# Optimization experiments

Measured on AMD Instinct MI355X. Metric: run time of the kernel, lower is better.

The kernel has to match this reference:

```python
import jax, jax.numpy as jnp
import numpy as np

B, S, D = 4096, 200, 64
EPS = 1e-3  # keras BatchNormalization default epsilon

def setup_inputs() -> dict:
    key = jax.random.key(0)
    ks = jax.random.split(key, 8)
    return {
        "em": jax.random.normal(ks[0], (B, D), jnp.float32),
        "eu": jax.random.normal(ks[1], (B, D), jnp.float32),
        "Xu": jax.random.normal(ks[2], (B, S, D), jnp.float32),
        "W1": jax.random.normal(ks[3], (4 * D, 64), jnp.float32) * 0.05,
        "b1": jnp.zeros((64,), jnp.float32),
        "W2": jax.random.normal(ks[4], (64, 32), jnp.float32) * 0.1,
        "b2": jnp.zeros((32,), jnp.float32),
        "W3": jax.random.normal(ks[5], (32, 1), jnp.float32) * 0.1,
        "b3": jnp.zeros((1,), jnp.float32),
        "gamma": jnp.ones((2 * D,), jnp.float32),
        "beta": jnp.zeros((2 * D,), jnp.float32),
        "mov_mean": jnp.zeros((2 * D,), jnp.float32),
        "mov_var": jnp.ones((2 * D,), jnp.float32),
    }

def reference(em, eu, Xu, W1, b1, W2, b2, W3, b3, gamma, beta, mov_mean, mov_var):
    # DIN attention: query = em tiled over seq, key = value = Xu
    q = jnp.broadcast_to(em[:, None, :], Xu.shape)            # [B,S,D]
    info = jnp.concatenate([q, Xu, q - Xu, q * Xu], axis=-1)  # [B,S,4D]
    h = jax.nn.relu(info @ W1 + b1)                           # [B,S,64]
    h = jax.nn.relu(h @ W2 + b2)                              # [B,S,32]
    logits = (h @ W3 + b3)[..., 0]                            # [B,S]
    w = jax.nn.softmax(logits, axis=-1)                       # [B,S]
    pooled = jnp.einsum('bs,bsd->bd', w, Xu)                  # [B,D]
    info_all = jnp.concatenate([pooled, em], axis=-1)         # [B,2D]
    bn = (info_all - mov_mean) * jax.lax.rsqrt(mov_var + EPS) * gamma + beta
    return jnp.concatenate([bn, eu], axis=-1)                 # [B,2D+Du]
```

## Files before the change

kernel.cpp:

```cpp
#include <hip/hip_runtime.h>
#include <hip/hip_bf16.h>
#include <math.h>

typedef __bf16 bf16_t;
typedef bf16_t bf16x2 __attribute__((ext_vector_type(2)));
typedef bf16_t bf16x8 __attribute__((ext_vector_type(8)));
typedef float  f32x4  __attribute__((ext_vector_type(4)));
typedef int    i32x4  __attribute__((ext_vector_type(4)));
typedef unsigned int u32;

#define SEQ 200
#define DD  64

#define MFMA(a, b, c) __builtin_amdgcn_mfma_f32_16x16x32_bf16((a), (b), (c), 0, 0, 0)

__global__ __launch_bounds__(256) void prep_kernel(
    const float* __restrict__ W1, const float* __restrict__ W2,
    bf16_t* __restrict__ Wbc, bf16_t* __restrict__ W1dt,
    bf16_t* __restrict__ W2t, float* __restrict__ W1sT)
{
  const int tid = threadIdx.x;
  for (int i = tid; i < 64 * 64; i += 256) {
    int n = i >> 6, k = i & 63;
    Wbc[i]  = (bf16_t)(W1[(64 + k) * 64 + n] - W1[(128 + k) * 64 + n]);
    W1dt[i] = (bf16_t)(W1[(192 + k) * 64 + n]);
    W1sT[i] = W1[k * 64 + n] + W1[(128 + k) * 64 + n];
  }
  for (int i = tid; i < 32 * 64; i += 256) {
    int n = i >> 6, k = i & 63;
    W2t[i] = (bf16_t)(W2[k * 32 + n]);
  }
}

__device__ __forceinline__ u32 pk2(float x, float y) {
  bf16x2 t;
  t[0] = (bf16_t)fmaxf(x, 0.f);
  t[1] = (bf16_t)fmaxf(y, 0.f);
  return __builtin_bit_cast(u32, t);
}

#define XR4(v) { v += __shfl_xor(v, 1); v += __shfl_xor(v, 2); \
                 v += __shfl_xor(v, 4); v += __shfl_xor(v, 8); }
#define XM4(v) { v = fmaxf(v, __shfl_xor(v, 1)); v = fmaxf(v, __shfl_xor(v, 2)); \
                 v = fmaxf(v, __shfl_xor(v, 4)); v = fmaxf(v, __shfl_xor(v, 8)); }

#define LOADT(t, Y0, Y1, Y2, Y3) do {                                          \
    int row_ = 16 * (t) + l16;                                                 \
    row_ = row_ < SEQ ? row_ : (SEQ - 1);                                      \
    const float4* p_ = Xr + (row_ * 16 + 2 * g);                               \
    Y0 = p_[0]; Y1 = p_[1]; Y2 = p_[8]; Y3 = p_[9];                            \
  } while (0)

#define PROC(MASKED, Y0, Y1, Y2, Y3) do {                                      \
    bf16x8 a0_, a1_;                                                           \
    a0_[0]=(bf16_t)Y0.x; a0_[1]=(bf16_t)Y0.y; a0_[2]=(bf16_t)Y0.z; a0_[3]=(bf16_t)Y0.w; \
    a0_[4]=(bf16_t)Y1.x; a0_[5]=(bf16_t)Y1.y; a0_[6]=(bf16_t)Y1.z; a0_[7]=(bf16_t)Y1.w; \
    a1_[0]=(bf16_t)Y2.x; a1_[1]=(bf16_t)Y2.y; a1_[2]=(bf16_t)Y2.z; a1_[3]=(bf16_t)Y2.w; \
    a1_[4]=(bf16_t)Y3.x; a1_[5]=(bf16_t)Y3.y; a1_[6]=(bf16_t)Y3.z; a1_[7]=(bf16_t)Y3.w; \
    f32x4 zz_ = {0.f, 0.f, 0.f, 0.f};                                          \
    f32x4 c0_ = MFMA(bB00, a0_, zz_); c0_ = MFMA(bB01, a1_, c0_);              \
    f32x4 c1_ = MFMA(bB10, a0_, zz_); c1_ = MFMA(bB11, a1_, c1_);              \
    f32x4 c2_ = MFMA(bB20, a0_, zz_); c2_ = MFMA(bB21, a1_, c2_);              \
    f32x4 c3_ = MFMA(bB30, a0_, zz_); c3_ = MFMA(bB31, a1_, c3_);              \
    u32 p00_ = pk2(c0_[0] + Q00, c0_[1] + Q01);                                \
    u32 p01_ = pk2(c0_[2] + Q02, c0_[3] + Q03);                                \
    u32 p10_ = pk2(c1_[0] + Q10, c1_[1] + Q11);                                \
    u32 p11_ = pk2(c1_[2] + Q12, c1_[3] + Q13);                                \
    u32 p20_ = pk2(c2_[0] + Q20, c2_[1] + Q21);                                \
    u32 p21_ = pk2(c2_[2] + Q22, c2_[3] + Q23);                                \
    u32 p30_ = pk2(c3_[0] + Q30, c3_[1] + Q31);                                \
    u32 p31_ = pk2(c3_[2] + Q32, c3_[3] + Q33);                                \
    u32 a00_ = __shfl(p00_, sl0), a01_ = __shfl(p01_, sl0);                    \
    u32 a10_ = __shfl(p10_, sl0), a11_ = __shfl(p11_, sl0);                    \
    u32 a20_ = __shfl(p20_, sl0), a21_ = __shfl(p21_, sl0);                    \
    u32 a30_ = __shfl(p30_, sl0), a31_ = __shfl(p31_, sl0);                    \
    u32 b00_ = __shfl(p00_, sl1), b01_ = __shfl(p01_, sl1);                    \
    u32 b10_ = __shfl(p10_, sl1), b11_ = __shfl(p11_, sl1);                    \
    u32 b20_ = __shfl(p20_, sl1), b21_ = __shfl(p21_, sl1);                    \
    u32 b30_ = __shfl(p30_, sl1), b31_ = __shfl(p31_, sl1);                    \
    i32x4 f0_ = { (int)(ghi ? a10_ : a00_), (int)(ghi ? a11_ : a01_),          \
                  (int)(ghi ? b10_ : b00_), (int)(ghi ? b11_ : b01_) };        \
    i32x4 f1_ = { (int)(ghi ? a30_ : a20_), (int)(ghi ? a31_ : a21_),          \
                  (int)(ghi ? b30_ : b20_), (int)(ghi ? b31_ : b21_) };        \
    bf16x8 hf0_ = __builtin_bit_cast(bf16x8, f0_);                             \
    bf16x8 hf1_ = __builtin_bit_cast(bf16x8, f1_);                             \
    f32x4 d0_ = MFMA(hf0_, W2f00, zz_); d0_ = MFMA(hf1_, W2f10, d0_);          \
    f32x4 d1_ = MFMA(hf0_, W2f01, zz_); d1_ = MFMA(hf1_, W2f11, d1_);          \
    float pr0_ = fmaxf(d0_[0] + b2v0, 0.f) * w3v0 + fmaxf(d1_[0] + b2v1, 0.f) * w3v1; \
    float pr1_ = fmaxf(d0_[1] + b2v0, 0.f) * w3v0 + fmaxf(d1_[1] + b2v1, 0.f) * w3v1; \
    float pr2_ = fmaxf(d0_[2] + b2v0, 0.f) * w3v0 + fmaxf(d1_[2] + b2v1, 0.f) * w3v1; \
    float pr3_ = fmaxf(d0_[3] + b2v0, 0.f) * w3v0 + fmaxf(d1_[3] + b2v1, 0.f) * w3v1; \
    XR4(pr0_) XR4(pr1_) XR4(pr2_) XR4(pr3_)                                    \
    float pv_ = pr0_;                                                          \
    pv_ = (s3 == 1) ? pr1_ : pv_;                                              \
    pv_ = (s3 == 2) ? pr2_ : pv_;                                              \
    pv_ = (s3 == 3) ? pr3_ : pv_;                                              \
    float lv_ = __shfl(pv_, lsrc) + b3s;                                       \
    if (MASKED && l16 >= 8) lv_ = -INFINITY;                                   \
    float tm_ = lv_;                                                           \
    XM4(tm_)                                                                   \
    float mn_ = fmaxf(m, tm_);                                                 \
    float al_ = __expf(m - mn_);                                               \
    float ee_ = __expf(lv_ - mn_);                                             \
    float S_ = ee_;                                                            \
    XR4(S_)                                                                    \
    Z = Z * al_ + S_;                                                          \
    Pa0 = Pa0 * al_ + ee_ * (float)a0_[0]; Pa1 = Pa1 * al_ + ee_ * (float)a0_[1]; \
    Pa2 = Pa2 * al_ + ee_ * (float)a0_[2]; Pa3 = Pa3 * al_ + ee_ * (float)a0_[3]; \
    Pa4 = Pa4 * al_ + ee_ * (float)a0_[4]; Pa5 = Pa5 * al_ + ee_ * (float)a0_[5]; \
    Pa6 = Pa6 * al_ + ee_ * (float)a0_[6]; Pa7 = Pa7 * al_ + ee_ * (float)a0_[7]; \
    Pb0 = Pb0 * al_ + ee_ * (float)a1_[0]; Pb1 = Pb1 * al_ + ee_ * (float)a1_[1]; \
    Pb2 = Pb2 * al_ + ee_ * (float)a1_[2]; Pb3 = Pb3 * al_ + ee_ * (float)a1_[3]; \
    Pb4 = Pb4 * al_ + ee_ * (float)a1_[4]; Pb5 = Pb5 * al_ + ee_ * (float)a1_[5]; \
    Pb6 = Pb6 * al_ + ee_ * (float)a1_[6]; Pb7 = Pb7 * al_ + ee_ * (float)a1_[7]; \
    m = mn_;                                                                   \
  } while (0)

__global__ __launch_bounds__(256, 3) void din_kernel(
    const float* __restrict__ em, const float* __restrict__ eu,
    const float* __restrict__ Xu, const float* __restrict__ b1,
    const float* __restrict__ b2, const float* __restrict__ W3,
    const float* __restrict__ b3, const float* __restrict__ gam,
    const float* __restrict__ bet, const float* __restrict__ mmean,
    const float* __restrict__ mvar, const bf16_t* __restrict__ Wbc,
    const bf16_t* __restrict__ W1dt, const bf16_t* __restrict__ W2t,
    const float* __restrict__ W1sT, float* __restrict__ out, int Btot)
{
  const int tid  = threadIdx.x;
  const int lane = tid & 63;
  const int wid  = tid >> 6;
  const int g    = lane >> 4;
  const int l16  = lane & 15;
  const int b    = blockIdx.x * 4 + wid;
  if (b >= Btot) return;

  const int  sl0  = 32 * (g & 1) + l16;
  const int  sl1  = sl0 + 16;
  const bool ghi  = (g >> 1) != 0;
  const int  s3   = l16 & 3;
  const int  lsrc = ((l16 >> 2) << 4) | s3;

  const float* emr  = em + (size_t)b * DD;
  const float  em_l = emr[lane];
  float4 ef0 = *(const float4*)&emr[8 * g];
  float4 ef1 = *(const float4*)&emr[8 * g + 4];
  float4 ef2 = *(const float4*)&emr[32 + 8 * g];
  float4 ef3 = *(const float4*)&emr[32 + 8 * g + 4];

  const bf16x8* Wbc8  = (const bf16x8*)Wbc;
  const bf16x8* W1dt8 = (const bf16x8*)W1dt;
  const bf16x8* W2t8  = (const bf16x8*)W2t;
#define MKBB(NAME, J, C, E0, E1)                                               \
  bf16x8 NAME; {                                                               \
    bf16x8 w_ = Wbc8[(16 * (J) + l16) * 8 + 4 * (C) + g];                      \
    bf16x8 d_ = W1dt8[(16 * (J) + l16) * 8 + 4 * (C) + g];                     \
    NAME[0] = (bf16_t)((float)w_[0] + E0.x * (float)d_[0]);                    \
    NAME[1] = (bf16_t)((float)w_[1] + E0.y * (float)d_[1]);                    \
    NAME[2] = (bf16_t)((float)w_[2] + E0.z * (float)d_[2]);                    \
    NAME[3] = (bf16_t)((float)w_[3] + E0.w * (float)d_[3]);                    \
    NAME[4] = (bf16_t)((float)w_[4] + E1.x * (float)d_[4]);                    \
    NAME[5] = (bf16_t)((float)w_[5] + E1.y * (float)d_[5]);                    \
    NAME[6] = (bf16_t)((float)w_[6] + E1.z * (float)d_[6]);                    \
    NAME[7] = (bf16_t)((float)w_[7] + E1.w * (float)d_[7]);                    \
  }
  MKBB(bB00, 0, 0, ef0, ef1) MKBB(bB01, 0, 1, ef2, ef3)
  MKBB(bB10, 1, 0, ef0, ef1) MKBB(bB11, 1, 1, ef2, ef3)
  MKBB(bB20, 2, 0, ef0, ef1) MKBB(bB21, 2, 1, ef2, ef3)
  MKBB(bB30, 3, 0, ef0, ef1) MKBB(bB31, 3, 1, ef2, ef3)
#undef MKBB

  const bf16x8 W2f00 = W2t8[(16 * 0 + l16) * 8 + 4 * 0 + g];
  const bf16x8 W2f01 = W2t8[(16 * 1 + l16) * 8 + 4 * 0 + g];
  const bf16x8 W2f10 = W2t8[(16 * 0 + l16) * 8 + 4 * 1 + g];
  const bf16x8 W2f11 = W2t8[(16 * 1 + l16) * 8 + 4 * 1 + g];

  const float b2v0 = b2[l16], b2v1 = b2[16 + l16];
  const float w3v0 = W3[l16], w3v1 = W3[16 + l16];
  const float b3s  = b3[0];

  float q = b1[lane];
  {
    const float4* wq = (const float4*)(W1sT + lane * 64);
    #pragma unroll
    for (int dd = 0; dd < 16; ++dd) {
      float4 wv = wq[dd];
      float ex = __shfl(em_l, 4 * dd + 0);
      float ey = __shfl(em_l, 4 * dd + 1);
      float ez = __shfl(em_l, 4 * dd + 2);
      float ew = __shfl(em_l, 4 * dd + 3);
      q += ex * wv.x + ey * wv.y + ez * wv.z + ew * wv.w;
    }
  }
#define MKQ(NAME, J, R) const float NAME = __shfl(q, 16 * (J) + 4 * g + (R));
  MKQ(Q00, 0, 0) MKQ(Q01, 0, 1) MKQ(Q02, 0, 2) MKQ(Q03, 0, 3)
  MKQ(Q10, 1, 0) MKQ(Q11, 1, 1) MKQ(Q12, 1, 2) MKQ(Q13, 1, 3)
  MKQ(Q20, 2, 0) MKQ(Q21, 2, 1) MKQ(Q22, 2, 2) MKQ(Q23, 2, 3)
  MKQ(Q30, 3, 0) MKQ(Q31, 3, 1) MKQ(Q32, 3, 2) MKQ(Q33, 3, 3)
#undef MKQ

  float m = -INFINITY, Z = 0.f;
  float Pa0 = 0.f, Pa1 = 0.f, Pa2 = 0.f, Pa3 = 0.f;
  float Pa4 = 0.f, Pa5 = 0.f, Pa6 = 0.f, Pa7 = 0.f;
  float Pb0 = 0.f, Pb1 = 0.f, Pb2 = 0.f, Pb3 = 0.f;
  float Pb4 = 0.f, Pb5 = 0.f, Pb6 = 0.f, Pb7 = 0.f;

  const float4* Xr = (const float4*)(Xu + (size_t)b * SEQ * DD);

  float4 A0, A1, A2, A3, B0, B1, B2, B3;
  LOADT(0, A0, A1, A2, A3);
  #pragma unroll 1
  for (int t = 0; t < 12; t += 2) {
    LOADT(t + 1, B0, B1, B2, B3);
    PROC(0, A0, A1, A2, A3);
    LOADT(t + 2, A0, A1, A2, A3);
    PROC(0, B0, B1, B2, B3);
  }
  PROC(1, A0, A1, A2, A3);

  XR4(Pa0) XR4(Pa1) XR4(Pa2) XR4(Pa3) XR4(Pa4) XR4(Pa5) XR4(Pa6) XR4(Pa7)
  XR4(Pb0) XR4(Pb1) XR4(Pb2) XR4(Pb3) XR4(Pb4) XR4(Pb5) XR4(Pb6) XR4(Pb7)
  const float invZ = 1.f / Z;

  const int  gsrc = (lane >> 3) & 3;
  const int  srcl = 16 * gsrc + l16;
  const int  esel = lane & 7;
  const bool hi   = lane >= 32;
  float pooled = 0.f, t_;
  t_ = __shfl(Pa0, srcl); if (!hi && esel == 0) pooled = t_;
  t_ = __shfl(Pa1, srcl); if (!hi && esel == 1) pooled = t_;
  t_ = __shfl(Pa2, srcl); if (!hi && esel == 2) pooled = t_;
  t_ = __shfl(Pa3, srcl); if (!hi && esel == 3) pooled = t_;
  t_ = __shfl(Pa4, srcl); if (!hi && esel == 4) pooled = t_;
  t_ = __shfl(Pa5, srcl); if (!hi && esel == 5) pooled = t_;
  t_ = __shfl(Pa6, srcl); if (!hi && esel == 6) pooled = t_;
  t_ = __shfl(Pa7, srcl); if (!hi && esel == 7) pooled = t_;
  t_ = __shfl(Pb0, srcl); if (hi && esel == 0) pooled = t_;
  t_ = __shfl(Pb1, srcl); if (hi && esel == 1) pooled = t_;
  t_ = __shfl(Pb2, srcl); if (hi && esel == 2) pooled = t_;
  t_ = __shfl(Pb3, srcl); if (hi && esel == 3) pooled = t_;
  t_ = __shfl(Pb4, srcl); if (hi && esel == 4) pooled = t_;
  t_ = __shfl(Pb5, srcl); if (hi && esel == 5) pooled = t_;
  t_ = __shfl(Pb6, srcl); if (hi && esel == 6) pooled = t_;
  t_ = __shfl(Pb7, srcl); if (hi && esel == 7) pooled = t_;
  pooled *= invZ;

  float o0 = (pooled - mmean[lane]) * rsqrtf(mvar[lane] + 1e-3f) * gam[lane] + bet[lane];
  float o1 = (em_l - mmean[64 + lane]) * rsqrtf(mvar[64 + lane] + 1e-3f) * gam[64 + lane] + bet[64 + lane];
  float o2 = eu[(size_t)b * 64 + lane];
  float* ob = out + (size_t)b * 192;
  ob[lane]       = o0;
  ob[64 + lane]  = o1;
  ob[128 + lane] = o2;
}

extern "C" void kernel_launch(void* const* d_in, const int* in_sizes, int n_in,
                              void* d_out, int out_size, void* d_ws, size_t ws_size,
                              hipStream_t stream) {
  const float* em = (const float*)d_in[0];
  const float* eu = (const float*)d_in[1];
  const float* Xu = (const float*)d_in[2];
  const float* W1 = (const float*)d_in[3];
  const float* b1 = (const float*)d_in[4];
  const float* W2 = (const float*)d_in[5];
  const float* b2 = (const float*)d_in[6];
  const float* W3 = (const float*)d_in[7];
  const float* b3 = (const float*)d_in[8];
  const float* ga = (const float*)d_in[9];
  const float* be = (const float*)d_in[10];
  const float* mm = (const float*)d_in[11];
  const float* mv = (const float*)d_in[12];
  int B = in_sizes[0] / DD;

  float*  W1sT = (float*)d_ws;
  bf16_t* Wbc  = (bf16_t*)((char*)d_ws + 64 * 64 * 4);
  bf16_t* W1dt = Wbc + 64 * 64;
  bf16_t* W2t  = W1dt + 64 * 64;

  prep_kernel<<<1, 256, 0, stream>>>(W1, W2, Wbc, W1dt, W2t, W1sT);
  din_kernel<<<(B + 3) / 4, 256, 0, stream>>>(em, eu, Xu, b1, b2, W3, b3, ga, be,
                                              mm, mv, Wbc, W1dt, W2t, W1sT,
                                              (float*)d_out, B);
}
```

Before: 349.9 us.

## Permute W1 columns to skip MFMA output shuffles and use lazy softmax rescale

Reorders the precomputed W1 columns so the first MFMA's output fragments already match the A-operand layout for the second MFMA. This removes the 16 cross-lane shuffles and selects per tile. The second MFMA's operands are swapped, so the W3 dot product reduces with two xor shuffles instead of four XR4 reductions plus a select and gather. The online softmax now rescales its accumulators only when some logit exceeds the running max by more than 8, and the per-lane Z reduction is deferred to the end. The wave-wide vote adds a branch, and the lazy threshold lets exponentials grow to about e^8, which is safe in fp32.

```diff
diff --git a/kernel.cpp b/kernel.cpp
--- a/kernel.cpp
+++ b/kernel.cpp
@@ -21,10 +21,12 @@
 {
   const int tid = threadIdx.x;
   for (int i = tid; i < 64 * 64; i += 256) {
-    int n = i >> 6, k = i & 63;
+    int rp = i >> 6, k = i & 63;
+    int j = rp >> 4, mm = rp & 15;
+    int n = ((j & 1) << 2) | ((j >> 1) << 5) | ((mm >> 2) << 3) | (mm & 3);
     Wbc[i]  = (bf16_t)(W1[(64 + k) * 64 + n] - W1[(128 + k) * 64 + n]);
     W1dt[i] = (bf16_t)(W1[(192 + k) * 64 + n]);
-    W1sT[i] = W1[k * 64 + n] + W1[(128 + k) * 64 + n];
+    W1sT[i] = W1[k * 64 + rp] + W1[(128 + k) * 64 + rp];
   }
   for (int i = tid; i < 32 * 64; i += 256) {
     int n = i >> 6, k = i & 63;
@@ -62,58 +64,52 @@
     f32x4 c1_ = MFMA(bB10, a0_, zz_); c1_ = MFMA(bB11, a1_, c1_);              \
     f32x4 c2_ = MFMA(bB20, a0_, zz_); c2_ = MFMA(bB21, a1_, c2_);              \
     f32x4 c3_ = MFMA(bB30, a0_, zz_); c3_ = MFMA(bB31, a1_, c3_);              \
-    u32 p00_ = pk2(c0_[0] + Q00, c0_[1] + Q01);                                \
-    u32 p01_ = pk2(c0_[2] + Q02, c0_[3] + Q03);                                \
-    u32 p10_ = pk2(c1_[0] + Q10, c1_[1] + Q11);                                \
-    u32 p11_ = pk2(c1_[2] + Q12, c1_[3] + Q13);                                \
-    u32 p20_ = pk2(c2_[0] + Q20, c2_[1] + Q21);                                \
-    u32 p21_ = pk2(c2_[2] + Q22, c2_[3] + Q23);                                \
-    u32 p30_ = pk2(c3_[0] + Q30, c3_[1] + Q31);                                \
-    u32 p31_ = pk2(c3_[2] + Q32, c3_[3] + Q33);                                \
-    u32 a00_ = __shfl(p00_, sl0), a01_ = __shfl(p01_, sl0);                    \
-    u32 a10_ = __shfl(p10_, sl0), a11_ = __shfl(p11_, sl0);                    \
-    u32 a20_ = __shfl(p20_, sl0), a21_ = __shfl(p21_, sl0);                    \
-    u32 a30_ = __shfl(p30_, sl0), a31_ = __shfl(p31_, sl0);                    \
-    u32 b00_ = __shfl(p00_, sl1), b01_ = __shfl(p01_, sl1);                    \
-    u32 b10_ = __shfl(p10_, sl1), b11_ = __shfl(p11_, sl1);                    \
-    u32 b20_ = __shfl(p20_, sl1), b21_ = __shfl(p21_, sl1);                    \
-    u32 b30_ = __shfl(p30_, sl1), b31_ = __shfl(p31_, sl1);                    \
-    i32x4 f0_ = { (int)(ghi ? a10_ : a00_), (int)(ghi ? a11_ : a01_),          \
-                  (int)(ghi ? b10_ : b00_), (int)(ghi ? b11_ : b01_) };        \
-    i32x4 f1_ = { (int)(ghi ? a30_ : a20_), (int)(ghi ? a31_ : a21_),          \
-                  (int)(ghi ? b30_ : b20_), (int)(ghi ? b31_ : b21_) };        \
+    i32x4 f0_ = { (int)pk2(c0_[0] + Q00, c0_[1] + Q01),                        \
+                  (int)pk2(c0_[2] + Q02, c0_[3] + Q03),                        \
+                  (int)pk2(c1_[0] + Q10, c1_[1] + Q11),                        \
+                  (int)pk2(c1_[2] + Q12, c1_[3] + Q13) };                      \
+    i32x4 f1_ = { (int)pk2(c2_[0] + Q20, c2_[1] + Q21),                        \
+                  (int)pk2(c2_[2] + Q22, c2_[3] + Q23),                        \
+                  (int)pk2(c3_[0] + Q30, c3_[1] + Q31),                        \
+                  (int)pk2(c3_[2] + Q32, c3_[3] + Q33) };                      \
     bf16x8 hf0_ = __builtin_bit_cast(bf16x8, f0_);                             \
     bf16x8 hf1_ = __builtin_bit_cast(bf16x8, f1_);                             \
-    f32x4 d0_ = MFMA(hf0_, W2f00, zz_); d0_ = MFMA(hf1_, W2f10, d0_);          \
-    f32x4 d1_ = MFMA(hf0_, W2f01, zz_); d1_ = MFMA(hf1_, W2f11, d1_);          \
-    float pr0_ = fmaxf(d0_[0] + b2v0, 0.f) * w3v0 + fmaxf(d1_[0] + b2v1, 0.f) * w3v1; \
-    float pr1_ = fmaxf(d0_[1] + b2v0, 0.f) * w3v0 + fmaxf(d1_[1] + b2v1, 0.f) * w3v1; \
-    float pr2_ = fmaxf(d0_[2] + b2v0, 0.f) * w3v0 + fmaxf(d1_[2] + b2v1, 0.f) * w3v1; \
-    float pr3_ = fmaxf(d0_[3] + b2v0, 0.f) * w3v0 + fmaxf(d1_[3] + b2v1, 0.f) * w3v1; \
-    XR4(pr0_) XR4(pr1_) XR4(pr2_) XR4(pr3_)                                    \
-    float pv_ = pr0_;                                                          \
-    pv_ = (s3 == 1) ? pr1_ : pv_;                                              \
-    pv_ = (s3 == 2) ? pr2_ : pv_;                                              \
-    pv_ = (s3 == 3) ? pr3_ : pv_;                                              \
-    float lv_ = __shfl(pv_, lsrc) + b3s;                                       \
+    f32x4 d0_ = MFMA(W2fA0, hf0_, zz_); d0_ = MFMA(W2fA1, hf1_, d0_);          \
+    f32x4 d1_ = MFMA(W2fB0, hf0_, zz_); d1_ = MFMA(W2fB1, hf1_, d1_);          \
+    float pr_ = fmaxf(d0_[0] + b2lo.x, 0.f) * w3lo.x                           \
+              + fmaxf(d0_[1] + b2lo.y, 0.f) * w3lo.y                           \
+              + fmaxf(d0_[2] + b2lo.z, 0.f) * w3lo.z                           \
+              + fmaxf(d0_[3] + b2lo.w, 0.f) * w3lo.w                           \
+              + fmaxf(d1_[0] + b2hi.x, 0.f) * w3hi.x                           \
+              + fmaxf(d1_[1] + b2hi.y, 0.f) * w3hi.y                           \
+              + fmaxf(d1_[2] + b2hi.z, 0.f) * w3hi.z                           \
+              + fmaxf(d1_[3] + b2hi.w, 0.f) * w3hi.w;                          \
+    pr_ += __shfl_xor(pr_, 16);                                                \
+    pr_ += __shfl_xor(pr_, 32);                                                \
+    float lv_ = pr_ + b3s;                                                     \
     if (MASKED && l16 >= 8) lv_ = -INFINITY;                                   \
-    float tm_ = lv_;                                                           \
-    XM4(tm_)                                                                   \
-    float mn_ = fmaxf(m, tm_);                                                 \
-    float al_ = __expf(m - mn_);                                               \
-    float ee_ = __expf(lv_ - mn_);                                             \
-    float S_ = ee_;                                                            \
-    XR4(S_)                                                                    \
-    Z = Z * al_ + S_;                                                          \
-    Pa0 = Pa0 * al_ + ee_ * (float)a0_[0]; Pa1 = Pa1 * al_ + ee_ * (float)a0_[1]; \
-    Pa2 = Pa2 * al_ + ee_ * (float)a0_[2]; Pa3 = Pa3 * al_ + ee_ * (float)a0_[3]; \
-    Pa4 = Pa4 * al_ + ee_ * (float)a0_[4]; Pa5 = Pa5 * al_ + ee_ * (float)a0_[5]; \
-    Pa6 = Pa6 * al_ + ee_ * (float)a0_[6]; Pa7 = Pa7 * al_ + ee_ * (float)a0_[7]; \
-    Pb0 = Pb0 * al_ + ee_ * (float)a1_[0]; Pb1 = Pb1 * al_ + ee_ * (float)a1_[1]; \
-    Pb2 = Pb2 * al_ + ee_ * (float)a1_[2]; Pb3 = Pb3 * al_ + ee_ * (float)a1_[3]; \
-    Pb4 = Pb4 * al_ + ee_ * (float)a1_[4]; Pb5 = Pb5 * al_ + ee_ * (float)a1_[5]; \
-    Pb6 = Pb6 * al_ + ee_ * (float)a1_[6]; Pb7 = Pb7 * al_ + ee_ * (float)a1_[7]; \
-    m = mn_;                                                                   \
+    if (!__all(lv_ <= m + 8.f)) {        \
+      float tm_ = lv_;                                                         \
+      XM4(tm_)                                                                 \
+      float mn_ = fmaxf(m, tm_);                                               \
+      float al_ = __expf(m - mn_);                                             \
+      Zp *= al_;                                                               \
+      Pa0 *= al_; Pa1 *= al_; Pa2 *= al_; Pa3 *= al_;                          \
+      Pa4 *= al_; Pa5 *= al_; Pa6 *= al_; Pa7 *= al_;                          \
+      Pb0 *= al_; Pb1 *= al_; Pb2 *= al_; Pb3 *= al_;                          \
+      Pb4 *= al_; Pb5 *= al_; Pb6 *= al_; Pb7 *= al_;                          \
+      m = mn_;                                                                 \
+    }                                                                          \
+    float ee_ = __expf(lv_ - m);                                               \
+    Zp += ee_;                                                                 \
+    Pa0 += ee_ * (float)a0_[0]; Pa1 += ee_ * (float)a0_[1];                    \
+    Pa2 += ee_ * (float)a0_[2]; Pa3 += ee_ * (float)a0_[3];                    \
+    Pa4 += ee_ * (float)a0_[4]; Pa5 += ee_ * (float)a0_[5];                    \
+    Pa6 += ee_ * (float)a0_[6]; Pa7 += ee_ * (float)a0_[7];                    \
+    Pb0 += ee_ * (float)a1_[0]; Pb1 += ee_ * (float)a1_[1];                    \
+    Pb2 += ee_ * (float)a1_[2]; Pb3 += ee_ * (float)a1_[3];                    \
+    Pb4 += ee_ * (float)a1_[4]; Pb5 += ee_ * (float)a1_[5];                    \
+    Pb6 += ee_ * (float)a1_[6]; Pb7 += ee_ * (float)a1_[7];                    \
   } while (0)
 
 __global__ __launch_bounds__(256, 3) void din_kernel(
@@ -134,12 +130,6 @@
   const int b    = blockIdx.x * 4 + wid;
   if (b >= Btot) return;
 
-  const int  sl0  = 32 * (g & 1) + l16;
-  const int  sl1  = sl0 + 16;
-  const bool ghi  = (g >> 1) != 0;
-  const int  s3   = l16 & 3;
-  const int  lsrc = ((l16 >> 2) << 4) | s3;
-
   const float* emr  = em + (size_t)b * DD;
   const float  em_l = emr[lane];
   float4 ef0 = *(const float4*)&emr[8 * g];
@@ -169,14 +159,16 @@
   MKBB(bB30, 3, 0, ef0, ef1) MKBB(bB31, 3, 1, ef2, ef3)
 #undef MKBB
 
-  const bf16x8 W2f00 = W2t8[(16 * 0 + l16) * 8 + 4 * 0 + g];
-  const bf16x8 W2f01 = W2t8[(16 * 1 + l16) * 8 + 4 * 0 + g];
-  const bf16x8 W2f10 = W2t8[(16 * 0 + l16) * 8 + 4 * 1 + g];
-  const bf16x8 W2f11 = W2t8[(16 * 1 + l16) * 8 + 4 * 1 + g];
-
-  const float b2v0 = b2[l16], b2v1 = b2[16 + l16];
-  const float w3v0 = W3[l16], w3v1 = W3[16 + l16];
-  const float b3s  = b3[0];
+  const bf16x8 W2fA0 = W2t8[l16 * 8 + g];
+  const bf16x8 W2fA1 = W2t8[l16 * 8 + 4 + g];
+  const bf16x8 W2fB0 = W2t8[(16 + l16) * 8 + g];
+  const bf16x8 W2fB1 = W2t8[(16 + l16) * 8 + 4 + g];
+
+  const float4 b2lo = *(const float4*)&b2[4 * g];
+  const float4 b2hi = *(const float4*)&b2[16 + 4 * g];
+  const float4 w3lo = *(const float4*)&W3[4 * g];
+  const float4 w3hi = *(const float4*)&W3[16 + 4 * g];
+  const float  b3s  = b3[0];
 
   float q = b1[lane];
   {
@@ -191,14 +183,14 @@
       q += ex * wv.x + ey * wv.y + ez * wv.z + ew * wv.w;
     }
   }
-#define MKQ(NAME, J, R) const float NAME = __shfl(q, 16 * (J) + 4 * g + (R));
+#define MKQ(NAME, J, R) const float NAME = __shfl(q, (((J)&1)<<2) + (((J)>>1)<<5) + 8*g + (R));
   MKQ(Q00, 0, 0) MKQ(Q01, 0, 1) MKQ(Q02, 0, 2) MKQ(Q03, 0, 3)
   MKQ(Q10, 1, 0) MKQ(Q11, 1, 1) MKQ(Q12, 1, 2) MKQ(Q13, 1, 3)
   MKQ(Q20, 2, 0) MKQ(Q21, 2, 1) MKQ(Q22, 2, 2) MKQ(Q23, 2, 3)
   MKQ(Q30, 3, 0) MKQ(Q31, 3, 1) MKQ(Q32, 3, 2) MKQ(Q33, 3, 3)
 #undef MKQ
 
-  float m = -INFINITY, Z = 0.f;
+  float m = -INFINITY, Zp = 0.f;
   float Pa0 = 0.f, Pa1 = 0.f, Pa2 = 0.f, Pa3 = 0.f;
   float Pa4 = 0.f, Pa5 = 0.f, Pa6 = 0.f, Pa7 = 0.f;
   float Pb0 = 0.f, Pb1 = 0.f, Pb2 = 0.f, Pb3 = 0.f;
@@ -217,9 +209,11 @@
   }
   PROC(1, A0, A1, A2, A3);
 
+  float Z = Zp;
+  XR4(Z)
+  const float invZ = 1.f / Z;
   XR4(Pa0) XR4(Pa1) XR4(Pa2) XR4(Pa3) XR4(Pa4) XR4(Pa5) XR4(Pa6) XR4(Pa7)
   XR4(Pb0) XR4(Pb1) XR4(Pb2) XR4(Pb3) XR4(Pb4) XR4(Pb5) XR4(Pb6) XR4(Pb7)
-  const float invZ = 1.f / Z;
 
   const int  gsrc = (lane >> 3) & 3;
   const int  srcl = 16 * gsrc + l16;
```

Measured after the change: 333.6 us. 1.05x faster.
